# Optimization experiments

Hardware: AMD Instinct MI355X
Metric: run time of the kernel (lower is better)

## Reference

```python
import jax, jax.numpy as jnp
import numpy as np

B = 65536
D_EMB = 512      # embedding_dim
D_SPD = 1        # speed_dim
D_LAT = 128      # speed_latent_dim
H = 256          # hidden_size
K = 6            # num_branch
D_IN = D_EMB + D_LAT  # 640, branch/speed-head input dim


def _lin(key, din, dout):
    kw, kb = jax.random.split(key)
    W = jax.random.normal(kw, (din, dout), dtype=jnp.float32) * 0.02
    b = jax.random.normal(kb, (dout,), dtype=jnp.float32) * 0.02
    return W, b


def setup_inputs() -> dict:
    key = jax.random.key(0)
    ks = jax.random.split(key, 16)
    embedding = jax.random.normal(ks[0], (B, D_EMB), dtype=jnp.float32)
    speed = jax.random.uniform(ks[1], (B, D_SPD), dtype=jnp.float32)
    command = jax.random.randint(ks[2], (B,), 1, K + 1, dtype=jnp.int32)  # values 1..6
    # speed input MLP: speed_dim -> H -> D_LAT
    Wsi1, bsi1 = _lin(ks[3], D_SPD, H)
    Wsi2, bsi2 = _lin(ks[4], H, D_LAT)
    # speed prediction head: D_IN -> H -> H -> speed_dim
    Wso1, bso1 = _lin(ks[5], D_IN, H)
    Wso2, bso2 = _lin(ks[6], H, H)
    Wso3, bso3 = _lin(ks[7], H, D_SPD)
    # K branch heads, stacked on leading axis: D_IN -> H -> H -> 3, sigmoid
    def _stack(key, din, dout):
        kw, kb = jax.random.split(key)
        W = jax.random.normal(kw, (K, din, dout), dtype=jnp.float32) * 0.02
        b = jax.random.normal(kb, (K, dout), dtype=jnp.float32) * 0.02
        return W, b
    Wb1, bb1 = _stack(ks[8], D_IN, H)
    Wb2, bb2 = _stack(ks[9], H, H)
    Wb3, bb3 = _stack(ks[10], H, 3)
    return dict(embedding=embedding, speed=speed, command=command,
                Wsi1=Wsi1, bsi1=bsi1, Wsi2=Wsi2, bsi2=bsi2,
                Wso1=Wso1, bso1=bso1, Wso2=Wso2, bso2=bso2, Wso3=Wso3, bso3=bso3,
                Wb1=Wb1, bb1=bb1, Wb2=Wb2, bb2=bb2, Wb3=Wb3, bb3=bb3)


def reference(embedding, speed, command,
              Wsi1, bsi1, Wsi2, bsi2,
              Wso1, bso1, Wso2, bso2, Wso3, bso3,
              Wb1, bb1, Wb2, bb2, Wb3, bb3):
    # speed -> latent
    sp = jax.nn.relu(speed @ Wsi1 + bsi1) @ Wsi2 + bsi2          # [B, D_LAT]
    emb = jnp.concatenate([embedding, sp], axis=1)               # [B, D_IN]
    # compute ALL K branch heads (as the original does), then mask by command
    h = jax.nn.relu(jnp.einsum('bd,kdh->bkh', emb, Wb1) + bb1)   # [B, K, H]
    h = jax.nn.relu(jnp.einsum('bkh,khj->bkj', h, Wb2) + bb2)    # [B, K, H]
    ctrl_all = jax.nn.sigmoid(jnp.einsum('bkh,kho->bko', h, Wb3) + bb3)  # [B, K, 3]
    mask = (command[:, None] - 1 == jnp.arange(K)[None, :]).astype(ctrl_all.dtype)  # [B, K]
    control_pred = jnp.sum(ctrl_all * mask[:, :, None], axis=1)  # [B, 3]
    # speed prediction head
    hs = jax.nn.relu(emb @ Wso1 + bso1)
    hs = jax.nn.relu(hs @ Wso2 + bso2)
    speed_pred = hs @ Wso3 + bso3                                # [B, 1]
    return control_pred, speed_pred
```

## Files before the change

### kernel.cpp

```cpp
#include <hip/hip_runtime.h>
#include <hip/hip_bf16.h>


#define NB 65536
#define NBRB 1030

typedef __attribute__((ext_vector_type(8))) short short8;
typedef __attribute__((ext_vector_type(4))) float f32x4;
typedef unsigned short bhalf;
typedef unsigned int u32;

__device__ __forceinline__ bhalf f2b(float x) {
    __hip_bfloat16 h = __float2bfloat16(x);
    return *reinterpret_cast<bhalf*>(&h);
}
__device__ __forceinline__ void gll16(const void* g, void* l) {
    __builtin_amdgcn_global_load_lds(
        (const __attribute__((address_space(1))) u32*)g,
        (__attribute__((address_space(3))) u32*)l, 16, 0, 0);
}
__device__ __forceinline__ int sadr(int row, int cb) {
    return row * 64 + (cb ^ (((row >> 1) & 3) << 4));
}
__device__ __forceinline__ int yadr(int row, int cb) {
    return row * 512 + (cb ^ ((row & 7) << 4));
}
__device__ __forceinline__ void wvm6() { asm volatile("s_waitcnt vmcnt(6)" ::: "memory"); }
__device__ __forceinline__ void wvm4() { asm volatile("s_waitcnt vmcnt(4)" ::: "memory"); }
__device__ __forceinline__ void wlgkm0() { asm volatile("s_waitcnt lgkmcnt(0)" ::: "memory"); }

__global__ __launch_bounds__(256) void k_wprep(
    const float* __restrict__ Wsi2, const float* __restrict__ Wso1,
    const float* __restrict__ Wso2, const float* __restrict__ Wb1,
    const float* __restrict__ Wb2,
    bhalf* __restrict__ Wsi2T, bhalf* __restrict__ Wso1T,
    bhalf* __restrict__ Wso2T, bhalf* __restrict__ Wb1T,
    bhalf* __restrict__ Wb2T) {
    __shared__ float T[64][65];
    const int id = blockIdx.x, t = threadIdx.x;
    const float* src; bhalf* dst; int K, N, tk, tn, b;
    if (id < 8)        { src = Wsi2; dst = Wsi2T; K = 256; N = 128; b = 0; int tl = id;      tk = tl / 2; tn = tl % 2; }
    else if (id < 48)  { src = Wso1; dst = Wso1T; K = 640; N = 256; b = 0; int tl = id - 8;  tk = tl / 4; tn = tl % 4; }
    else if (id < 64)  { src = Wso2; dst = Wso2T; K = 256; N = 256; b = 0; int tl = id - 48; tk = tl / 4; tn = tl % 4; }
    else if (id < 304) { src = Wb1;  dst = Wb1T;  K = 640; N = 256; int li = id - 64;  b = li / 40; int tl = li % 40; tk = tl / 4; tn = tl % 4; }
    else               { src = Wb2;  dst = Wb2T;  K = 256; N = 256; int li = id - 304; b = li / 16; int tl = li % 16; tk = tl / 4; tn = tl % 4; }
    const int k0 = tk * 64, n0 = tn * 64;
    src += (size_t)b * K * N; dst += (size_t)b * N * K;
    const int c = t & 63, r0 = t >> 6;
#pragma unroll
    for (int j = 0; j < 16; ++j) {
        int r = r0 + j * 4;
        T[r][c] = src[(size_t)(k0 + r) * N + n0 + c];
    }
    __syncthreads();
#pragma unroll
    for (int j = 0; j < 16; ++j) {
        int r = r0 + j * 4;
        dst[(size_t)(n0 + r) * K + k0 + c] = f2b(T[c][r]);
    }
}

__global__ __launch_bounds__(256) void k_prep(
    const float* __restrict__ speed, const float* __restrict__ Wsi1,
    const float* __restrict__ bsi1, const bhalf* __restrict__ Wsi2T,
    const float* __restrict__ bsi2, const int* __restrict__ cmd,
    bhalf* __restrict__ spb, int* __restrict__ bcnt) {
    __shared__ bhalf A[64 * 72];
    __shared__ bhalf BT[128 * 72];
    const int t = threadIdx.x, lane = t & 63, wid = t >> 6;
    const int rbase = blockIdx.x * 64;
    if (wid == 0) {
        int c = cmd[rbase + lane] - 1;
        int v = 0;
#pragma unroll
        for (int g = 0; g < 6; ++g) {
            unsigned long long m = __ballot(c == g);
            if (lane == g) v = (int)__popcll(m);
        }
        if (lane < 6) bcnt[blockIdx.x * 6 + lane] = v;
    }
    const int wm = wid >> 1, wn = wid & 1;
    f32x4 acc[2][4];
    for (int m = 0; m < 2; ++m) for (int n = 0; n < 4; ++n)
        for (int r = 0; r < 4; ++r) acc[m][n][r] = 0.f;
    const int ar = t >> 2, kp = (t & 3) * 16;
    const float s = speed[rbase + ar];
    for (int kc = 0; kc < 4; ++kc) {
        short8 w0, w1;
#pragma unroll
        for (int j = 0; j < 8; ++j) {
            int k = kc * 64 + kp + j;
            w0[j] = (short)f2b(fmaxf(fmaf(s, Wsi1[k], bsi1[k]), 0.f));
            w1[j] = (short)f2b(fmaxf(fmaf(s, Wsi1[k + 8], bsi1[k + 8]), 0.f));
        }
        *(short8*)&A[ar * 72 + kp] = w0;
        *(short8*)&A[ar * 72 + kp + 8] = w1;
#pragma unroll
        for (int j = 0; j < 4; ++j) {
            int ch = t + j * 256;
            int n2 = ch >> 3, ko = (ch & 7) * 8;
            *(short8*)&BT[n2 * 72 + ko] =
                *(const short8*)(Wsi2T + n2 * 256 + kc * 64 + ko);
        }
        __syncthreads();
#pragma unroll
        for (int ks = 0; ks < 2; ++ks) {
            short8 a[2], b[4];
#pragma unroll
            for (int m = 0; m < 2; ++m)
                a[m] = *(const short8*)&A[(wm * 32 + m * 16 + (lane & 15)) * 72 + ks * 32 + (lane >> 4) * 8];
#pragma unroll
            for (int n = 0; n < 4; ++n)
                b[n] = *(const short8*)&BT[(wn * 64 + n * 16 + (lane & 15)) * 72 + ks * 32 + (lane >> 4) * 8];
#pragma unroll
            for (int m = 0; m < 2; ++m)
#pragma unroll
                for (int n = 0; n < 4; ++n)
                    acc[m][n] = __builtin_amdgcn_mfma_f32_16x16x32_bf16(a[m], b[n], acc[m][n], 0, 0, 0);
        }
        __syncthreads();
    }
#pragma unroll
    for (int m = 0; m < 2; ++m)
#pragma unroll
    for (int n = 0; n < 4; ++n) {
        int col = wn * 64 + n * 16 + (lane & 15);
        float bias = bsi2[col];
#pragma unroll
        for (int r = 0; r < 4; ++r) {
            int row = rbase + wm * 32 + m * 16 + (lane >> 4) * 4 + r;
            spb[row * 128 + col] = f2b(acc[m][n][r] + bias);
        }
    }
}

__global__ __launch_bounds__(1024) void k_scan(
    const int* __restrict__ bcnt, int* __restrict__ chunkoff,
    int* __restrict__ pad) {
    __shared__ int sc[1024];
    __shared__ int tot[8];
    __shared__ int spo[8];
    const int t = threadIdx.x;
    for (int g = 0; g < 6; ++g) {
        int v = bcnt[t * 6 + g];
        sc[t] = v;
        __syncthreads();
        for (int s = 1; s < 1024; s <<= 1) {
            int u = (t >= s) ? sc[t - s] : 0;
            __syncthreads();
            sc[t] += u;
            __syncthreads();
        }
        if (t == 1023) tot[g] = sc[t];
        chunkoff[t * 6 + g] = sc[t] - v;
        __syncthreads();
    }
    if (t == 0) {
        int off = 0;
        for (int g = 0; g < 6; ++g) {
            spo[g] = off; pad[g] = off; pad[8 + g] = tot[g];
            off += ((tot[g] + 63) >> 6) << 6;
        }
        spo[6] = off; pad[6] = off;
    }
    __syncthreads();
    for (int g = 0; g < 6; ++g) chunkoff[t * 6 + g] += spo[g];
}

__global__ __launch_bounds__(256) void k_scatter(
    const int* __restrict__ cmd, const int* __restrict__ chunkoff,
    int* __restrict__ perm) {
    const int lane = threadIdx.x & 63, w = threadIdx.x >> 6;
    const int chunk = blockIdx.x * 4 + w;
    const int idx = chunk * 64 + lane;
    const int c = cmd[idx] - 1;
#pragma unroll
    for (int g = 0; g < 6; ++g) {
        unsigned long long m = __ballot(c == g);
        if (c == g) {
            int pos = chunkoff[chunk * 6 + g] + (int)__popcll(m & ((1ull << lane) - 1ull));
            perm[pos] = idx;
        }
    }
}

__global__ __launch_bounds__(256, 3) void k_head(
    const float* __restrict__ emb, const bhalf* __restrict__ spb,
    const bhalf* __restrict__ Wso1T, const float* __restrict__ bso1,
    const bhalf* __restrict__ Wso2T, const float* __restrict__ bso2,
    const float* __restrict__ Wso3, const float* __restrict__ bso3,
    const bhalf* __restrict__ Wb1T, const float* __restrict__ bb1,
    const bhalf* __restrict__ Wb2T, const float* __restrict__ bb2,
    const float* __restrict__ Wb3, const float* __restrict__ bb3,
    const int* __restrict__ pad, const int* __restrict__ perm,
    float* __restrict__ out) {
    __shared__ __align__(16) char SA[2][8192];
    __shared__ __align__(16) char Yb[32768];
    const int t = threadIdx.x, lane = t & 63, wid = t >> 6;
    const bool isB = blockIdx.x < NBRB;
    int tstart, DOUT, gcnt, gbase;
    const bhalf *W1T, *W2T; const float *b1, *b2, *W3, *b3;
    if (isB) {
        tstart = blockIdx.x * 64;
        if (tstart >= pad[6]) return;
        int g = 0;
        while (pad[g + 1] <= tstart) ++g;
        gbase = pad[g]; gcnt = pad[8 + g];
        W1T = Wb1T + (size_t)g * (256 * 640); b1 = bb1 + g * 256;
        W2T = Wb2T + (size_t)g * (256 * 256); b2 = bb2 + g * 256;
        W3  = Wb3  + (size_t)g * (256 * 3);   b3 = bb3 + g * 3;
        DOUT = 3;
    } else {
        tstart = (blockIdx.x - NBRB) * 64;
        gbase = 0; gcnt = NB;
        W1T = Wso1T; b1 = bso1; W2T = Wso2T; b2 = bso2; W3 = Wso3; b3 = bso3;
        DOUT = 1;
    }

    const int rowA0 = t >> 3, rowA1 = rowA0 + 32, rowS = t >> 2;
    int ra0, ra1, raS;
    if (isB) {
        int p0 = tstart + rowA0, p1 = tstart + rowA1, pS = tstart + rowS;
        ra0 = ((p0 - gbase) < gcnt) ? perm[p0] : 0;
        ra1 = ((p1 - gbase) < gcnt) ? perm[p1] : 0;
        raS = ((pS - gbase) < gcnt) ? perm[pS] : 0;
    } else {
        ra0 = tstart + rowA0; ra1 = tstart + rowA1; raS = tstart + rowS;
    }
    const int lcA0 = ((t & 7) * 16) ^ ((rowA0 & 7) << 4);
    const int lcA1 = ((t & 7) * 16) ^ ((rowA1 & 7) << 4);
    const int lcS  = ((t & 3) * 16) ^ (((rowS >> 1) & 3) << 4);
    const char* embp0 = (const char*)(emb + (size_t)ra0 * 512);
    const char* embp1 = (const char*)(emb + (size_t)ra1 * 512);
    const char* spbp  = (const char*)(spb + (size_t)raS * 128);
    const int dstA = t * 16;

#define ST_A(KN, BUF) do { int kn_ = (KN); char* d_ = &SA[BUF][0] + dstA;        \
        if (kn_ < 16) {                                                           \
            gll16(embp0 + kn_ * 128 + lcA0, d_);                                  \
            gll16(embp1 + kn_ * 128 + lcA1, d_ + 4096);                           \
        } else {                                                                  \
            gll16(spbp + (kn_ - 16) * 64 + lcS, d_);                              \
            gll16(spbp + (kn_ - 16) * 64 + lcS, d_ + 4096);                       \
        } } while (0)

    const int arow = lane & 15, koff = (lane >> 4) * 16;
    const int kb = (lane >> 4) * 16;
    const char* bp0 = (const char*)W1T + (size_t)(wid * 64 + 0  + arow) * 1280 + kb;
    const char* bp1 = (const char*)W1T + (size_t)(wid * 64 + 16 + arow) * 1280 + kb;
    const char* bp2 = (const char*)W1T + (size_t)(wid * 64 + 32 + arow) * 1280 + kb;
    const char* bp3 = (const char*)W1T + (size_t)(wid * 64 + 48 + arow) * 1280 + kb;

    float bi1[4], bi2[4];
#pragma unroll
    for (int n = 0; n < 4; ++n) {
        bi1[n] = b1[wid * 64 + n * 16 + arow];
        bi2[n] = b2[wid * 64 + n * 16 + arow];
    }

    f32x4 acc[4][4];
#pragma unroll
    for (int m = 0; m < 4; ++m)
#pragma unroll
        for (int n = 0; n < 4; ++n)
#pragma unroll
            for (int r = 0; r < 4; ++r) acc[m][n][r] = 0.f;

    ST_A(0, 0);
    for (int kc = 0; kc < 20; ++kc) {
        const int buf = kc & 1;
        short8 b0 = *(const short8*)(bp0 + kc * 64);
        short8 b1f = *(const short8*)(bp1 + kc * 64);
        short8 b2f = *(const short8*)(bp2 + kc * 64);
        short8 b3f = *(const short8*)(bp3 + kc * 64);
        if (kc < 19) { ST_A(kc + 1, buf ^ 1); wvm6(); }
        else         { wvm4(); }
        __builtin_amdgcn_s_barrier();
        const char* SAc = &SA[buf][0];
        short8 a[4];
        if (kc < 16) {
#pragma unroll
            for (int m = 0; m < 4; ++m) {
                int row = m * 16 + arow;
                int sw = (row & 7) << 4;
                int c0 = (lane >> 4) * 32;
                float4 f0 = *(const float4*)(SAc + row * 128 + (c0 ^ sw));
                float4 f1 = *(const float4*)(SAc + row * 128 + ((c0 + 16) ^ sw));
                a[m][0] = (short)f2b(f0.x); a[m][1] = (short)f2b(f0.y);
                a[m][2] = (short)f2b(f0.z); a[m][3] = (short)f2b(f0.w);
                a[m][4] = (short)f2b(f1.x); a[m][5] = (short)f2b(f1.y);
                a[m][6] = (short)f2b(f1.z); a[m][7] = (short)f2b(f1.w);
            }
        } else {
#pragma unroll
            for (int m = 0; m < 4; ++m)
                a[m] = *(const short8*)(SAc + sadr(m * 16 + arow, koff));
        }
#pragma unroll
        for (int m = 0; m < 4; ++m) {
            acc[m][0] = __builtin_amdgcn_mfma_f32_16x16x32_bf16(a[m], b0,  acc[m][0], 0, 0, 0);
            acc[m][1] = __builtin_amdgcn_mfma_f32_16x16x32_bf16(a[m], b1f, acc[m][1], 0, 0, 0);
            acc[m][2] = __builtin_amdgcn_mfma_f32_16x16x32_bf16(a[m], b2f, acc[m][2], 0, 0, 0);
            acc[m][3] = __builtin_amdgcn_mfma_f32_16x16x32_bf16(a[m], b3f, acc[m][3], 0, 0, 0);
        }
        __builtin_amdgcn_s_barrier();
    }
#pragma unroll
    for (int m = 0; m < 4; ++m)
#pragma unroll
    for (int n = 0; n < 4; ++n) {
        int col = wid * 64 + n * 16 + arow;
#pragma unroll
        for (int r = 0; r < 4; ++r) {
            int row = m * 16 + (lane >> 4) * 4 + r;
            *(bhalf*)(Yb + yadr(row, 2 * col)) = f2b(fmaxf(acc[m][n][r] + bi1[n], 0.f));
            acc[m][n][r] = 0.f;
        }
    }
    wlgkm0();
    __builtin_amdgcn_s_barrier();
    {
        const char* cp0 = (const char*)W2T + (size_t)(wid * 64 + 0  + arow) * 512 + kb;
        const char* cp1 = (const char*)W2T + (size_t)(wid * 64 + 16 + arow) * 512 + kb;
        const char* cp2 = (const char*)W2T + (size_t)(wid * 64 + 32 + arow) * 512 + kb;
        const char* cp3 = (const char*)W2T + (size_t)(wid * 64 + 48 + arow) * 512 + kb;
        for (int kc = 0; kc < 8; ++kc) {
            short8 b0 = *(const short8*)(cp0 + kc * 64);
            short8 b1f = *(const short8*)(cp1 + kc * 64);
            short8 b2f = *(const short8*)(cp2 + kc * 64);
            short8 b3f = *(const short8*)(cp3 + kc * 64);
            short8 a[4];
#pragma unroll
            for (int m = 0; m < 4; ++m)
                a[m] = *(const short8*)(Yb + yadr(m * 16 + arow, kc * 64 + koff));
#pragma unroll
            for (int m = 0; m < 4; ++m) {
                acc[m][0] = __builtin_amdgcn_mfma_f32_16x16x32_bf16(a[m], b0,  acc[m][0], 0, 0, 0);
                acc[m][1] = __builtin_amdgcn_mfma_f32_16x16x32_bf16(a[m], b1f, acc[m][1], 0, 0, 0);
                acc[m][2] = __builtin_amdgcn_mfma_f32_16x16x32_bf16(a[m], b2f, acc[m][2], 0, 0, 0);
                acc[m][3] = __builtin_amdgcn_mfma_f32_16x16x32_bf16(a[m], b3f, acc[m][3], 0, 0, 0);
            }
        }
    }
    __builtin_amdgcn_s_barrier();
#pragma unroll
    for (int m = 0; m < 4; ++m)
#pragma unroll
    for (int n = 0; n < 4; ++n) {
        int col = wid * 64 + n * 16 + arow;
#pragma unroll
        for (int r = 0; r < 4; ++r) {
            int row = m * 16 + (lane >> 4) * 4 + r;
            *(bhalf*)(Yb + yadr(row, 2 * col)) = f2b(fmaxf(acc[m][n][r] + bi2[n], 0.f));
        }
    }
    wlgkm0();
    __builtin_amdgcn_s_barrier();
    f32x4 z;
#pragma unroll
    for (int r = 0; r < 4; ++r) z[r] = 0.f;
    const int col3 = arow;
    for (int kc = 0; kc < 8; ++kc) {
        short8 a3 = *(const short8*)(Yb + yadr(wid * 16 + arow, kc * 64 + koff));
        short8 bw;
#pragma unroll
        for (int j = 0; j < 8; ++j) bw[j] = 0;
        if (col3 < DOUT) {
            int kbq = kc * 32 + (lane >> 4) * 8;
#pragma unroll
            for (int j = 0; j < 8; ++j)
                bw[j] = (short)f2b(W3[(kbq + j) * DOUT + col3]);
        }
        z = __builtin_amdgcn_mfma_f32_16x16x32_bf16(a3, bw, z, 0, 0, 0);
    }
    if (col3 < DOUT) {
        float bias = b3[col3];
#pragma unroll
        for (int rr = 0; rr < 4; ++rr) {
            int r = wid * 16 + (lane >> 4) * 4 + rr;
            int p2 = tstart + r;
            if ((p2 - gbase) < gcnt) {
                float v = z[rr] + bias;
                if (isB) {
                    int ro = perm[p2];
                    out[(size_t)ro * 3 + col3] = 1.f / (1.f + __expf(-v));
                } else {
                    out[(size_t)NB * 3 + p2] = v;
                }
            }
        }
    }
#undef ST_A
}

extern "C" void kernel_launch(void* const* d_in, const int* in_sizes, int n_in,
                              void* d_out, int out_size, void* d_ws, size_t ws_size,
                              hipStream_t stream) {
    (void)in_sizes; (void)n_in; (void)out_size; (void)ws_size;
    const float* emb   = (const float*)d_in[0];
    const float* speed = (const float*)d_in[1];
    const int*   cmd   = (const int*)d_in[2];
    const float* Wsi1  = (const float*)d_in[3];
    const float* bsi1  = (const float*)d_in[4];
    const float* Wsi2  = (const float*)d_in[5];
    const float* bsi2  = (const float*)d_in[6];
    const float* Wso1  = (const float*)d_in[7];
    const float* bso1  = (const float*)d_in[8];
    const float* Wso2  = (const float*)d_in[9];
    const float* bso2  = (const float*)d_in[10];
    const float* Wso3  = (const float*)d_in[11];
    const float* bso3  = (const float*)d_in[12];
    const float* Wb1   = (const float*)d_in[13];
    const float* bb1   = (const float*)d_in[14];
    const float* Wb2   = (const float*)d_in[15];
    const float* bb2   = (const float*)d_in[16];
    const float* Wb3   = (const float*)d_in[17];
    const float* bb3   = (const float*)d_in[18];
    float* out = (float*)d_out;

    char* ws = (char*)d_ws;
    bhalf* spb      = (bhalf*)(ws);
    int*   perm     = (int*)(ws + 16777216);
    int*   bcnt     = (int*)(ws + 17040896);
    int*   chunkoff = (int*)(ws + 17065472);
    int*   pad      = (int*)(ws + 17090048);
    bhalf* Wsi2T    = (bhalf*)(ws + 17090304);
    bhalf* Wso1T    = (bhalf*)(ws + 17155840);
    bhalf* Wso2T    = (bhalf*)(ws + 17483520);
    bhalf* Wb1T     = (bhalf*)(ws + 17614592);
    bhalf* Wb2T     = (bhalf*)(ws + 19580672);

    k_wprep<<<400, 256, 0, stream>>>(Wsi2, Wso1, Wso2, Wb1, Wb2,
                                     Wsi2T, Wso1T, Wso2T, Wb1T, Wb2T);
    k_prep<<<NB / 64, 256, 0, stream>>>(speed, Wsi1, bsi1, Wsi2T, bsi2, cmd,
                                        spb, bcnt);
    k_scan<<<1, 1024, 0, stream>>>(bcnt, chunkoff, pad);
    k_scatter<<<NB / 256, 256, 0, stream>>>(cmd, chunkoff, perm);
    k_head<<<NBRB + NB / 64, 256, 0, stream>>>(emb, spb,
                                               Wso1T, bso1, Wso2T, bso2, Wso3, bso3,
                                               Wb1T, bb1, Wb2T, bb2, Wb3, bb3,
                                               pad, perm, out);
}
```

Baseline: 184.6 us.

## Fuse branch and speed heads into one persistent 512-thread kernel sharing A tiles

Replaces separate branch and speed-head blocks with a persistent 1024-block kernel of 512 threads, where waves 0-3 compute the selected branch head and waves 4-7 compute the speed head over the same permuted 64-row tile. Both heads share one LDS staging of the embedding/latent input, so each row's A data is loaded once instead of twice. It also prefetches the next weight fragments in registers during the first two GEMMs. In exchange it uses larger LDS (80KB) and more registers per block, and the speed head now runs in permuted row order.

```diff
diff --git a/kernel.cpp b/kernel.cpp
--- a/kernel.cpp
+++ b/kernel.cpp
@@ -3,7 +3,6 @@
 
 
 #define NB 65536
-#define NBRB 1030
 
 typedef __attribute__((ext_vector_type(8))) short short8;
 typedef __attribute__((ext_vector_type(4))) float f32x4;
@@ -22,12 +21,12 @@
 __device__ __forceinline__ int sadr(int row, int cb) {
     return row * 64 + (cb ^ (((row >> 1) & 3) << 4));
 }
-__device__ __forceinline__ int yadr(int row, int cb) {
-    return row * 512 + (cb ^ ((row & 7) << 4));
-}
-__device__ __forceinline__ void wvm6() { asm volatile("s_waitcnt vmcnt(6)" ::: "memory"); }
-__device__ __forceinline__ void wvm4() { asm volatile("s_waitcnt vmcnt(4)" ::: "memory"); }
-__device__ __forceinline__ void wlgkm0() { asm volatile("s_waitcnt lgkmcnt(0)" ::: "memory"); }
+__device__ __forceinline__ int yadr2(int row, int cb) {
+    return row * 1024 + (cb ^ ((row & 7) << 4));
+}
+__device__ __forceinline__ void wvm5()  { asm volatile("s_waitcnt vmcnt(5)"  ::: "memory"); }
+__device__ __forceinline__ void wvm0()  { asm volatile("s_waitcnt vmcnt(0)"  ::: "memory"); }
+__device__ __forceinline__ void wlgkm0(){ asm volatile("s_waitcnt lgkmcnt(0)" ::: "memory"); }
 
 __global__ __launch_bounds__(256) void k_wprep(
     const float* __restrict__ Wsi2, const float* __restrict__ Wso1,
@@ -184,7 +183,7 @@
     }
 }
 
-__global__ __launch_bounds__(256, 3) void k_head(
+__global__ __launch_bounds__(512, 2) void k3(
     const float* __restrict__ emb, const bhalf* __restrict__ spb,
     const bhalf* __restrict__ Wso1T, const float* __restrict__ bso1,
     const bhalf* __restrict__ Wso2T, const float* __restrict__ bso2,
@@ -194,203 +193,215 @@
     const float* __restrict__ Wb3, const float* __restrict__ bb3,
     const int* __restrict__ pad, const int* __restrict__ perm,
     float* __restrict__ out) {
-    __shared__ __align__(16) char SA[2][8192];
-    __shared__ __align__(16) char Yb[32768];
+    __shared__ __align__(16) char L[81920];
+    char* const SA0 = L;
+    char* const Yb  = L + 16384;
     const int t = threadIdx.x, lane = t & 63, wid = t >> 6;
-    const bool isB = blockIdx.x < NBRB;
-    int tstart, DOUT, gcnt, gbase;
-    const bhalf *W1T, *W2T; const float *b1, *b2, *W3, *b3;
-    if (isB) {
-        tstart = blockIdx.x * 64;
-        if (tstart >= pad[6]) return;
+    const int head = wid >> 2, wn = wid & 3;
+    const int pad6 = pad[6];
+    const int arow = lane & 15, kb = (lane >> 4) * 16;
+    const int rowA = t >> 3;
+    const int lcA = ((t & 7) * 16) ^ ((rowA & 7) << 4);
+    const int rowS = (t & 255) >> 2;
+    const int lcS = ((t & 3) * 16) ^ (((rowS >> 1) & 3) << 4);
+    const int dstA = t * 16;
+    const int spdst = (t < 256) ? (t * 16) : (4096 + (t - 256) * 16);
+
+    const bhalf* W1h = head ? Wso1T : Wb1T;
+    const bhalf* W2h = head ? Wso2T : Wb2T;
+    const float* b1h = head ? bso1 : bb1;
+    const float* b2h = head ? bso2 : bb2;
+    const float* W3h = head ? Wso3 : Wb3;
+    const float* b3h = head ? bso3 : bb3;
+    const int DOUT = head ? 1 : 3;
+    const int col0 = wn * 64 + arow;
+
+    for (int tile = blockIdx.x; tile * 64 < pad6; tile += 1024) {
+        const int tstart = tile * 64;
         int g = 0;
         while (pad[g + 1] <= tstart) ++g;
-        gbase = pad[g]; gcnt = pad[8 + g];
-        W1T = Wb1T + (size_t)g * (256 * 640); b1 = bb1 + g * 256;
-        W2T = Wb2T + (size_t)g * (256 * 256); b2 = bb2 + g * 256;
-        W3  = Wb3  + (size_t)g * (256 * 3);   b3 = bb3 + g * 3;
-        DOUT = 3;
-    } else {
-        tstart = (blockIdx.x - NBRB) * 64;
-        gbase = 0; gcnt = NB;
-        W1T = Wso1T; b1 = bso1; W2T = Wso2T; b2 = bso2; W3 = Wso3; b3 = bso3;
-        DOUT = 1;
-    }
-
-    const int rowA0 = t >> 3, rowA1 = rowA0 + 32, rowS = t >> 2;
-    int ra0, ra1, raS;
-    if (isB) {
-        int p0 = tstart + rowA0, p1 = tstart + rowA1, pS = tstart + rowS;
-        ra0 = ((p0 - gbase) < gcnt) ? perm[p0] : 0;
-        ra1 = ((p1 - gbase) < gcnt) ? perm[p1] : 0;
-        raS = ((pS - gbase) < gcnt) ? perm[pS] : 0;
-    } else {
-        ra0 = tstart + rowA0; ra1 = tstart + rowA1; raS = tstart + rowS;
-    }
-    const int lcA0 = ((t & 7) * 16) ^ ((rowA0 & 7) << 4);
-    const int lcA1 = ((t & 7) * 16) ^ ((rowA1 & 7) << 4);
-    const int lcS  = ((t & 3) * 16) ^ (((rowS >> 1) & 3) << 4);
-    const char* embp0 = (const char*)(emb + (size_t)ra0 * 512);
-    const char* embp1 = (const char*)(emb + (size_t)ra1 * 512);
-    const char* spbp  = (const char*)(spb + (size_t)raS * 128);
-    const int dstA = t * 16;
-
-#define ST_A(KN, BUF) do { int kn_ = (KN); char* d_ = &SA[BUF][0] + dstA;        \
-        if (kn_ < 16) {                                                           \
-            gll16(embp0 + kn_ * 128 + lcA0, d_);                                  \
-            gll16(embp1 + kn_ * 128 + lcA1, d_ + 4096);                           \
-        } else {                                                                  \
-            gll16(spbp + (kn_ - 16) * 64 + lcS, d_);                              \
-            gll16(spbp + (kn_ - 16) * 64 + lcS, d_ + 4096);                       \
-        } } while (0)
-
-    const int arow = lane & 15, koff = (lane >> 4) * 16;
-    const int kb = (lane >> 4) * 16;
-    const char* bp0 = (const char*)W1T + (size_t)(wid * 64 + 0  + arow) * 1280 + kb;
-    const char* bp1 = (const char*)W1T + (size_t)(wid * 64 + 16 + arow) * 1280 + kb;
-    const char* bp2 = (const char*)W1T + (size_t)(wid * 64 + 32 + arow) * 1280 + kb;
-    const char* bp3 = (const char*)W1T + (size_t)(wid * 64 + 48 + arow) * 1280 + kb;
-
-    float bi1[4], bi2[4];
-#pragma unroll
-    for (int n = 0; n < 4; ++n) {
-        bi1[n] = b1[wid * 64 + n * 16 + arow];
-        bi2[n] = b2[wid * 64 + n * 16 + arow];
-    }
-
-    f32x4 acc[4][4];
-#pragma unroll
-    for (int m = 0; m < 4; ++m)
-#pragma unroll
-        for (int n = 0; n < 4; ++n)
-#pragma unroll
-            for (int r = 0; r < 4; ++r) acc[m][n][r] = 0.f;
-
-    ST_A(0, 0);
-    for (int kc = 0; kc < 20; ++kc) {
-        const int buf = kc & 1;
-        short8 b0 = *(const short8*)(bp0 + kc * 64);
-        short8 b1f = *(const short8*)(bp1 + kc * 64);
-        short8 b2f = *(const short8*)(bp2 + kc * 64);
-        short8 b3f = *(const short8*)(bp3 + kc * 64);
-        if (kc < 19) { ST_A(kc + 1, buf ^ 1); wvm6(); }
-        else         { wvm4(); }
+        const int gbase = pad[g], gcnt = pad[8 + g];
+        const int goff = head ? 0 : g;
+        const bhalf* W1T = W1h + (size_t)goff * (256 * 640);
+        const bhalf* W2T = W2h + (size_t)goff * (256 * 256);
+        const float* b1p = b1h + goff * 256;
+        const float* b2p = b2h + goff * 256;
+        const float* W3p = W3h + (size_t)goff * (256 * 3);
+        const float* b3p = b3h + goff * 3;
+
+        const int pA = tstart + rowA;
+        const int rA = ((pA - gbase) < gcnt) ? perm[pA] : 0;
+        const int pS = tstart + rowS;
+        const int rS = ((pS - gbase) < gcnt) ? perm[pS] : 0;
+        const char* embp = (const char*)(emb + (size_t)rA * 512);
+        const char* spbp = (const char*)(spb + (size_t)rS * 128);
+        const char* bp1_0 = (const char*)W1T + (size_t)(col0 +  0) * 1280 + kb;
+        const char* bp1_1 = (const char*)W1T + (size_t)(col0 + 16) * 1280 + kb;
+        const char* bp1_2 = (const char*)W1T + (size_t)(col0 + 32) * 1280 + kb;
+        const char* bp1_3 = (const char*)W1T + (size_t)(col0 + 48) * 1280 + kb;
+
+        float bi1[4], bi2[4];
+#pragma unroll
+        for (int n = 0; n < 4; ++n) {
+            bi1[n] = b1p[col0 + n * 16];
+            bi2[n] = b2p[col0 + n * 16];
+        }
+
+        f32x4 acc[4][4];
+#pragma unroll
+        for (int m = 0; m < 4; ++m)
+#pragma unroll
+            for (int n = 0; n < 4; ++n)
+#pragma unroll
+                for (int r = 0; r < 4; ++r) acc[m][n][r] = 0.f;
+
+#define ST_A3(KN, BUF) do { int kn_ = (KN);                                      \
+        if (kn_ < 16) gll16(embp + kn_ * 128 + lcA, SA0 + (BUF) * 8192 + dstA);  \
+        else          gll16(spbp + (kn_ - 16) * 64 + lcS, SA0 + (BUF) * 8192 + spdst); \
+    } while (0)
+
+        short8 bc0 = *(const short8*)(bp1_0);
+        short8 bc1 = *(const short8*)(bp1_1);
+        short8 bc2 = *(const short8*)(bp1_2);
+        short8 bc3 = *(const short8*)(bp1_3);
+        ST_A3(0, 0);
+#pragma unroll 2
+        for (int kc = 0; kc < 20; ++kc) {
+            const int buf = kc & 1;
+            short8 bn0, bn1, bn2, bn3;
+            if (kc < 19) {
+                bn0 = *(const short8*)(bp1_0 + (kc + 1) * 64);
+                bn1 = *(const short8*)(bp1_1 + (kc + 1) * 64);
+                bn2 = *(const short8*)(bp1_2 + (kc + 1) * 64);
+                bn3 = *(const short8*)(bp1_3 + (kc + 1) * 64);
+                ST_A3(kc + 1, buf ^ 1);
+                wvm5();
+            } else {
+                wvm0();
+            }
+            __builtin_amdgcn_s_barrier();
+            const char* SAc = SA0 + buf * 8192;
+            short8 a[4];
+            if (kc < 16) {
+#pragma unroll
+                for (int m = 0; m < 4; ++m) {
+                    int row = m * 16 + arow;
+                    int sw = (row & 7) << 4;
+                    int c0 = (lane >> 4) * 32;
+                    float4 f0 = *(const float4*)(SAc + row * 128 + (c0 ^ sw));
+                    float4 f1 = *(const float4*)(SAc + row * 128 + ((c0 + 16) ^ sw));
+                    a[m][0] = (short)f2b(f0.x); a[m][1] = (short)f2b(f0.y);
+                    a[m][2] = (short)f2b(f0.z); a[m][3] = (short)f2b(f0.w);
+                    a[m][4] = (short)f2b(f1.x); a[m][5] = (short)f2b(f1.y);
+                    a[m][6] = (short)f2b(f1.z); a[m][7] = (short)f2b(f1.w);
+                }
+            } else {
+#pragma unroll
+                for (int m = 0; m < 4; ++m)
+                    a[m] = *(const short8*)(SAc + sadr(m * 16 + arow, kb));
+            }
+#pragma unroll
+            for (int m = 0; m < 4; ++m) {
+                acc[m][0] = __builtin_amdgcn_mfma_f32_16x16x32_bf16(a[m], bc0, acc[m][0], 0, 0, 0);
+                acc[m][1] = __builtin_amdgcn_mfma_f32_16x16x32_bf16(a[m], bc1, acc[m][1], 0, 0, 0);
+                acc[m][2] = __builtin_amdgcn_mfma_f32_16x16x32_bf16(a[m], bc2, acc[m][2], 0, 0, 0);
+                acc[m][3] = __builtin_amdgcn_mfma_f32_16x16x32_bf16(a[m], bc3, acc[m][3], 0, 0, 0);
+            }
+            if (kc < 19) { bc0 = bn0; bc1 = bn1; bc2 = bn2; bc3 = bn3; }
+            __builtin_amdgcn_s_barrier();
+        }
+        const char* bp2_0 = (const char*)W2T + (size_t)(col0 +  0) * 512 + kb;
+        const char* bp2_1 = (const char*)W2T + (size_t)(col0 + 16) * 512 + kb;
+        const char* bp2_2 = (const char*)W2T + (size_t)(col0 + 32) * 512 + kb;
+        const char* bp2_3 = (const char*)W2T + (size_t)(col0 + 48) * 512 + kb;
+        short8 c0 = *(const short8*)(bp2_0);
+        short8 c1 = *(const short8*)(bp2_1);
+        short8 c2 = *(const short8*)(bp2_2);
+        short8 c3 = *(const short8*)(bp2_3);
+#pragma unroll
+        for (int m = 0; m < 4; ++m)
+#pragma unroll
+        for (int n = 0; n < 4; ++n) {
+            int col = wid * 64 + n * 16 + arow;
+#pragma unroll
+            for (int r = 0; r < 4; ++r) {
+                int row = m * 16 + (lane >> 4) * 4 + r;
+                *(bhalf*)(Yb + yadr2(row, 2 * col)) = f2b(fmaxf(acc[m][n][r] + bi1[n], 0.f));
+                acc[m][n][r] = 0.f;
+            }
+        }
+        wlgkm0();
         __builtin_amdgcn_s_barrier();
-        const char* SAc = &SA[buf][0];
-        short8 a[4];
-        if (kc < 16) {
+        for (int kc = 0; kc < 8; ++kc) {
+            short8 d0, d1, d2, d3;
+            if (kc < 7) {
+                d0 = *(const short8*)(bp2_0 + (kc + 1) * 64);
+                d1 = *(const short8*)(bp2_1 + (kc + 1) * 64);
+                d2 = *(const short8*)(bp2_2 + (kc + 1) * 64);
+                d3 = *(const short8*)(bp2_3 + (kc + 1) * 64);
+            }
+            short8 a[4];
+#pragma unroll
+            for (int m = 0; m < 4; ++m)
+                a[m] = *(const short8*)(Yb + yadr2(m * 16 + arow, head * 512 + kc * 64 + kb));
 #pragma unroll
             for (int m = 0; m < 4; ++m) {
-                int row = m * 16 + arow;
-                int sw = (row & 7) << 4;
-                int c0 = (lane >> 4) * 32;
-                float4 f0 = *(const float4*)(SAc + row * 128 + (c0 ^ sw));
-                float4 f1 = *(const float4*)(SAc + row * 128 + ((c0 + 16) ^ sw));
-                a[m][0] = (short)f2b(f0.x); a[m][1] = (short)f2b(f0.y);
-                a[m][2] = (short)f2b(f0.z); a[m][3] = (short)f2b(f0.w);
-                a[m][4] = (short)f2b(f1.x); a[m][5] = (short)f2b(f1.y);
-                a[m][6] = (short)f2b(f1.z); a[m][7] = (short)f2b(f1.w);
-            }
-        } else {
-#pragma unroll
-            for (int m = 0; m < 4; ++m)
-                a[m] = *(const short8*)(SAc + sadr(m * 16 + arow, koff));
-        }
-#pragma unroll
-        for (int m = 0; m < 4; ++m) {
-            acc[m][0] = __builtin_amdgcn_mfma_f32_16x16x32_bf16(a[m], b0,  acc[m][0], 0, 0, 0);
-            acc[m][1] = __builtin_amdgcn_mfma_f32_16x16x32_bf16(a[m], b1f, acc[m][1], 0, 0, 0);
-            acc[m][2] = __builtin_amdgcn_mfma_f32_16x16x32_bf16(a[m], b2f, acc[m][2], 0, 0, 0);
-            acc[m][3] = __builtin_amdgcn_mfma_f32_16x16x32_bf16(a[m], b3f, acc[m][3], 0, 0, 0);
+                acc[m][0] = __builtin_amdgcn_mfma_f32_16x16x32_bf16(a[m], c0, acc[m][0], 0, 0, 0);
+                acc[m][1] = __builtin_amdgcn_mfma_f32_16x16x32_bf16(a[m], c1, acc[m][1], 0, 0, 0);
+                acc[m][2] = __builtin_amdgcn_mfma_f32_16x16x32_bf16(a[m], c2, acc[m][2], 0, 0, 0);
+                acc[m][3] = __builtin_amdgcn_mfma_f32_16x16x32_bf16(a[m], c3, acc[m][3], 0, 0, 0);
+            }
+            if (kc < 7) { c0 = d0; c1 = d1; c2 = d2; c3 = d3; }
         }
         __builtin_amdgcn_s_barrier();
-    }
-#pragma unroll
-    for (int m = 0; m < 4; ++m)
-#pragma unroll
-    for (int n = 0; n < 4; ++n) {
-        int col = wid * 64 + n * 16 + arow;
-#pragma unroll
-        for (int r = 0; r < 4; ++r) {
-            int row = m * 16 + (lane >> 4) * 4 + r;
-            *(bhalf*)(Yb + yadr(row, 2 * col)) = f2b(fmaxf(acc[m][n][r] + bi1[n], 0.f));
-            acc[m][n][r] = 0.f;
-        }
-    }
-    wlgkm0();
-    __builtin_amdgcn_s_barrier();
-    {
-        const char* cp0 = (const char*)W2T + (size_t)(wid * 64 + 0  + arow) * 512 + kb;
-        const char* cp1 = (const char*)W2T + (size_t)(wid * 64 + 16 + arow) * 512 + kb;
-        const char* cp2 = (const char*)W2T + (size_t)(wid * 64 + 32 + arow) * 512 + kb;
-        const char* cp3 = (const char*)W2T + (size_t)(wid * 64 + 48 + arow) * 512 + kb;
+#pragma unroll
+        for (int m = 0; m < 4; ++m)
+#pragma unroll
+        for (int n = 0; n < 4; ++n) {
+            int col = wid * 64 + n * 16 + arow;
+#pragma unroll
+            for (int r = 0; r < 4; ++r) {
+                int row = m * 16 + (lane >> 4) * 4 + r;
+                *(bhalf*)(Yb + yadr2(row, 2 * col)) = f2b(fmaxf(acc[m][n][r] + bi2[n], 0.f));
+            }
+        }
+        wlgkm0();
+        __builtin_amdgcn_s_barrier();
+        f32x4 z;
+#pragma unroll
+        for (int r = 0; r < 4; ++r) z[r] = 0.f;
+        const int col3 = arow;
+        const int rbase3 = wn * 16;
         for (int kc = 0; kc < 8; ++kc) {
-            short8 b0 = *(const short8*)(cp0 + kc * 64);
-            short8 b1f = *(const short8*)(cp1 + kc * 64);
-            short8 b2f = *(const short8*)(cp2 + kc * 64);
-            short8 b3f = *(const short8*)(cp3 + kc * 64);
-            short8 a[4];
-#pragma unroll
-            for (int m = 0; m < 4; ++m)
-                a[m] = *(const short8*)(Yb + yadr(m * 16 + arow, kc * 64 + koff));
-#pragma unroll
-            for (int m = 0; m < 4; ++m) {
-                acc[m][0] = __builtin_amdgcn_mfma_f32_16x16x32_bf16(a[m], b0,  acc[m][0], 0, 0, 0);
-                acc[m][1] = __builtin_amdgcn_mfma_f32_16x16x32_bf16(a[m], b1f, acc[m][1], 0, 0, 0);
-                acc[m][2] = __builtin_amdgcn_mfma_f32_16x16x32_bf16(a[m], b2f, acc[m][2], 0, 0, 0);
-                acc[m][3] = __builtin_amdgcn_mfma_f32_16x16x32_bf16(a[m], b3f, acc[m][3], 0, 0, 0);
-            }
-        }
-    }
-    __builtin_amdgcn_s_barrier();
-#pragma unroll
-    for (int m = 0; m < 4; ++m)
-#pragma unroll
-    for (int n = 0; n < 4; ++n) {
-        int col = wid * 64 + n * 16 + arow;
-#pragma unroll
-        for (int r = 0; r < 4; ++r) {
-            int row = m * 16 + (lane >> 4) * 4 + r;
-            *(bhalf*)(Yb + yadr(row, 2 * col)) = f2b(fmaxf(acc[m][n][r] + bi2[n], 0.f));
-        }
-    }
-    wlgkm0();
-    __builtin_amdgcn_s_barrier();
-    f32x4 z;
-#pragma unroll
-    for (int r = 0; r < 4; ++r) z[r] = 0.f;
-    const int col3 = arow;
-    for (int kc = 0; kc < 8; ++kc) {
-        short8 a3 = *(const short8*)(Yb + yadr(wid * 16 + arow, kc * 64 + koff));
-        short8 bw;
-#pragma unroll
-        for (int j = 0; j < 8; ++j) bw[j] = 0;
+            short8 a3 = *(const short8*)(Yb + yadr2(rbase3 + arow, head * 512 + kc * 64 + kb));
+            short8 bw;
+#pragma unroll
+            for (int j = 0; j < 8; ++j) bw[j] = 0;
+            if (col3 < DOUT) {
+                int kq = kc * 32 + (lane >> 4) * 8;
+#pragma unroll
+                for (int j = 0; j < 8; ++j)
+                    bw[j] = (short)f2b(W3p[(kq + j) * DOUT + col3]);
+            }
+            z = __builtin_amdgcn_mfma_f32_16x16x32_bf16(a3, bw, z, 0, 0, 0);
+        }
         if (col3 < DOUT) {
-            int kbq = kc * 32 + (lane >> 4) * 8;
-#pragma unroll
-            for (int j = 0; j < 8; ++j)
-                bw[j] = (short)f2b(W3[(kbq + j) * DOUT + col3]);
-        }
-        z = __builtin_amdgcn_mfma_f32_16x16x32_bf16(a3, bw, z, 0, 0, 0);
-    }
-    if (col3 < DOUT) {
-        float bias = b3[col3];
-#pragma unroll
-        for (int rr = 0; rr < 4; ++rr) {
-            int r = wid * 16 + (lane >> 4) * 4 + rr;
-            int p2 = tstart + r;
-            if ((p2 - gbase) < gcnt) {
-                float v = z[rr] + bias;
-                if (isB) {
+            float bias = b3p[col3];
+#pragma unroll
+            for (int rr = 0; rr < 4; ++rr) {
+                int r = rbase3 + (lane >> 4) * 4 + rr;
+                int p2 = tstart + r;
+                if ((p2 - gbase) < gcnt) {
                     int ro = perm[p2];
-                    out[(size_t)ro * 3 + col3] = 1.f / (1.f + __expf(-v));
-                } else {
-                    out[(size_t)NB * 3 + p2] = v;
+                    float v = z[rr] + bias;
+                    if (head == 0) out[(size_t)ro * 3 + col3] = 1.f / (1.f + __expf(-v));
+                    else           out[(size_t)NB * 3 + ro] = v;
                 }
             }
         }
-    }
-#undef ST_A
+        __builtin_amdgcn_s_barrier();
+#undef ST_A3
+    }
 }
 
 extern "C" void kernel_launch(void* const* d_in, const int* in_sizes, int n_in,
@@ -436,8 +447,8 @@
                                         spb, bcnt);
     k_scan<<<1, 1024, 0, stream>>>(bcnt, chunkoff, pad);
     k_scatter<<<NB / 256, 256, 0, stream>>>(cmd, chunkoff, perm);
-    k_head<<<NBRB + NB / 64, 256, 0, stream>>>(emb, spb,
-                                               Wso1T, bso1, Wso2T, bso2, Wso3, bso3,
-                                               Wb1T, bb1, Wb2T, bb2, Wb3, bb3,
-                                               pad, perm, out);
-}
+    k3<<<1024, 512, 0, stream>>>(emb, spb,
+                                 Wso1T, bso1, Wso2T, bso2, Wso3, bso3,
+                                 Wb1T, bb1, Wb2T, bb2, Wb3, bb3,
+                                 pad, perm, out);
+}
```

After: 377.2 us. +104.3%, slower.
